# Kernel tuning notes

Hardware: AMD Instinct MI355X
Metric: run time of the kernel (lower is better)

Reference implementation:

```python
import jax, jax.numpy as jnp
import numpy as np

N_NODES = 100000
N_EDGES = 2000000
N_GRAPHS = 1024
HIDDEN = 32
LATENT = 8


def setup_inputs() -> dict:
    key = jax.random.key(0)
    ks = jax.random.split(key, 12)
    x = jax.random.normal(ks[0], (N_NODES, 1), dtype=jnp.float32)
    edge_index = jax.random.randint(ks[1], (2, N_EDGES), 0, N_NODES, dtype=jnp.int32)
    batch = jnp.sort(jax.random.randint(ks[2], (N_NODES,), 0, N_GRAPHS, dtype=jnp.int32))
    s = 0.1
    W = jax.random.normal(ks[3], (1, HIDDEN), dtype=jnp.float32) * s
    b = jax.random.normal(ks[4], (HIDDEN,), dtype=jnp.float32) * s
    w_mu = jax.random.normal(ks[5], (HIDDEN, LATENT), dtype=jnp.float32) * s
    b_mu = jax.random.normal(ks[6], (LATENT,), dtype=jnp.float32) * s
    w_lv = jax.random.normal(ks[7], (HIDDEN, LATENT), dtype=jnp.float32) * s
    b_lv = jax.random.normal(ks[8], (LATENT,), dtype=jnp.float32) * s
    w_dec = jax.random.normal(ks[9], (LATENT, 100), dtype=jnp.float32) * s
    b_dec = jax.random.normal(ks[10], (100,), dtype=jnp.float32) * s
    eps = jax.random.normal(ks[11], (N_GRAPHS, LATENT), dtype=jnp.float32)
    return {"x": x, "edge_index": edge_index, "batch": batch, "W": W, "b": b,
            "w_mu": w_mu, "b_mu": b_mu, "w_lv": w_lv, "b_lv": b_lv,
            "w_dec": w_dec, "b_dec": b_dec, "eps": eps}


def gcn_conv(x, edge_index, W, b):
    # PyG GCNConv: add self-loops, symmetric D^-1/2 (A+I) D^-1/2 normalization
    n = x.shape[0]
    loop = jnp.arange(n, dtype=edge_index.dtype)
    src = jnp.concatenate([edge_index[0], loop])
    dst = jnp.concatenate([edge_index[1], loop])
    deg = jax.ops.segment_sum(jnp.ones_like(dst, dtype=x.dtype), dst, num_segments=n)
    dinv = jnp.where(deg > 0, jax.lax.rsqrt(jnp.maximum(deg, 1.0)), 0.0)
    norm = dinv[src] * dinv[dst]          # [E+N]
    h = x @ W                              # [N, hidden] (tiny GEMM)
    msg = h[src] * norm[:, None]           # gather + scale (memory bound)
    out = jax.ops.segment_sum(msg, dst, num_segments=n)  # scatter-add
    return out + b


def reference(x, edge_index, batch, W, b, w_mu, b_mu, w_lv, b_lv, w_dec, b_dec, eps):
    G = eps.shape[0]
    h = jax.nn.relu(gcn_conv(x, edge_index, W, b))       # [N, hidden]
    sums = jax.ops.segment_sum(h, batch, num_segments=G)
    cnts = jax.ops.segment_sum(jnp.ones((h.shape[0],), h.dtype), batch, num_segments=G)
    pooled = sums / jnp.maximum(cnts, 1.0)[:, None]      # global_mean_pool [G, hidden]
    mu = pooled @ w_mu + b_mu                            # [G, latent]
    logvar = pooled @ w_lv + b_lv
    z = mu + eps * jnp.exp(0.5 * logvar)                 # reparam
    adj_logits = (z @ w_dec + b_dec).reshape(-1, 10, 10)
    adj = (jax.nn.sigmoid(adj_logits) > 0.5).astype(jnp.float32)
    return adj, mu, logvar
```

## Files before the change

kernel.cpp:

```cpp
#include <hip/hip_runtime.h>

#define HID 32
#define LAT 8
#define BSH 8
#define BUCK 256
#define CAPSH 13
#define CB 512
#define PB 512
#define PEV 16
#define PCHUNK (PB * PEV)

__device__ __forceinline__ double atomAddF64(double* p, double v) {
    return unsafeAtomicAdd(p, v);
}

__global__ void zero_kernel(unsigned* __restrict__ p, int n) {
    int i = blockIdx.x * blockDim.x + threadIdx.x;
    if (i < n) p[i] = 0;
}


__global__ __launch_bounds__(PB)
void place3_kernel(const unsigned* __restrict__ src, const unsigned* __restrict__ dst,
                   int E, int HBn,
                   unsigned* __restrict__ cursor, unsigned* __restrict__ csr) {
    __shared__ unsigned cnt[512];
    __shared__ unsigned gbase[512];
    uint4 dv[PEV / 4];
    unsigned rank[PEV];
    int tid = threadIdx.x;

    cnt[tid] = 0;
    __syncthreads();

    int E4 = E >> 2;
    int base4 = blockIdx.x * (PCHUNK / 4);
    #pragma unroll
    for (int k = 0; k < PEV / 4; k++) {
        int i4 = base4 + k * PB + tid;
        if (i4 < E4) {
            dv[k] = ((const uint4*)dst)[i4];
            rank[4 * k + 0] = atomicAdd(&cnt[dv[k].x >> BSH], 1u);
            rank[4 * k + 1] = atomicAdd(&cnt[dv[k].y >> BSH], 1u);
            rank[4 * k + 2] = atomicAdd(&cnt[dv[k].z >> BSH], 1u);
            rank[4 * k + 3] = atomicAdd(&cnt[dv[k].w >> BSH], 1u);
        }
    }
    __syncthreads();

    if (tid < HBn) {
        unsigned c = cnt[tid];
        gbase[tid] = c ? atomicAdd(&cursor[tid], c) : 0u;
    }
    __syncthreads();

    #pragma unroll
    for (int k = 0; k < PEV / 4; k++) {
        int i4 = base4 + k * PB + tid;
        if (i4 < E4) {
            uint4 sv = ((const uint4*)src)[i4];
            unsigned d, s, bin, r;
            d = dv[k].x; s = sv.x; bin = d >> BSH; r = gbase[bin] + rank[4 * k + 0];
            if (r < (1u << CAPSH)) csr[((size_t)bin << CAPSH) + r] = ((d & (BUCK - 1u)) << 17) | s;
            d = dv[k].y; s = sv.y; bin = d >> BSH; r = gbase[bin] + rank[4 * k + 1];
            if (r < (1u << CAPSH)) csr[((size_t)bin << CAPSH) + r] = ((d & (BUCK - 1u)) << 17) | s;
            d = dv[k].z; s = sv.z; bin = d >> BSH; r = gbase[bin] + rank[4 * k + 2];
            if (r < (1u << CAPSH)) csr[((size_t)bin << CAPSH) + r] = ((d & (BUCK - 1u)) << 17) | s;
            d = dv[k].w; s = sv.w; bin = d >> BSH; r = gbase[bin] + rank[4 * k + 3];
            if (r < (1u << CAPSH)) csr[((size_t)bin << CAPSH) + r] = ((d & (BUCK - 1u)) << 17) | s;
        }
    }
}

__global__ __launch_bounds__(CB)
void bdeg_kernel(const unsigned* __restrict__ cursor, const unsigned* __restrict__ csr,
                 int N, int G,
                 const float* __restrict__ x, const int* __restrict__ batch,
                 float* __restrict__ dinv, float* __restrict__ y32,
                 int* __restrict__ startArr) {
    int b = blockIdx.x;
    __shared__ unsigned cnt[BUCK];
    if (threadIdx.x < BUCK) cnt[threadIdx.x] = 0;
    __syncthreads();
    unsigned n = min(cursor[b], (unsigned)(1u << CAPSH));
    const unsigned* seg = csr + ((size_t)b << CAPSH);
    unsigned n4 = n >> 2;
    for (unsigned i = threadIdx.x; i < n4; i += CB) {
        uint4 v = ((const uint4*)seg)[i];
        atomicAdd(&cnt[v.x >> 17], 1u);
        atomicAdd(&cnt[v.y >> 17], 1u);
        atomicAdd(&cnt[v.z >> 17], 1u);
        atomicAdd(&cnt[v.w >> 17], 1u);
    }
    unsigned t = (n4 << 2) + threadIdx.x;
    if (t < n) atomicAdd(&cnt[seg[t] >> 17], 1u);
    __syncthreads();
    if (threadIdx.x < BUCK) {
        int node = (b << BSH) + threadIdx.x;
        if (node < N) {
            double dv = 1.0 / sqrt((double)(cnt[threadIdx.x] + 1));
            dinv[node] = (float)dv;
            y32[node] = (float)((double)x[node] * dv);
            int b1 = batch[node];
            if (node == 0) { for (int g = 0; g <= b1; g++) startArr[g] = 0; }
            else { int bp = batch[node - 1]; for (int g = bp + 1; g <= b1; g++) startArr[g] = node; }
            if (node == N - 1) { for (int g = b1 + 1; g <= G; g++) startArr[g] = N; }
        }
    }
}

__global__ __launch_bounds__(CB)
void bsum_kernel(const unsigned* __restrict__ cursor, const unsigned* __restrict__ csr,
                 int N,
                 const float* __restrict__ dinv, const float* __restrict__ y32,
                 double* __restrict__ acc) {
    int b = blockIdx.x;
    __shared__ double accs[BUCK];
    if (threadIdx.x < BUCK) accs[threadIdx.x] = 0.0;
    __syncthreads();
    unsigned n = min(cursor[b], (unsigned)(1u << CAPSH));
    const unsigned* seg = csr + ((size_t)b << CAPSH);
    unsigned n4 = n >> 2;
    for (unsigned i = threadIdx.x; i < n4; i += CB) {
        uint4 v = ((const uint4*)seg)[i];
        float ya = y32[v.x & 0x1FFFFu];
        float yb = y32[v.y & 0x1FFFFu];
        float yc = y32[v.z & 0x1FFFFu];
        float yd = y32[v.w & 0x1FFFFu];
        atomicAdd(&accs[v.x >> 17], (double)ya);
        atomicAdd(&accs[v.y >> 17], (double)yb);
        atomicAdd(&accs[v.z >> 17], (double)yc);
        atomicAdd(&accs[v.w >> 17], (double)yd);
    }
    unsigned t = (n4 << 2) + threadIdx.x;
    if (t < n) {
        unsigned v = seg[t];
        atomicAdd(&accs[v >> 17], (double)y32[v & 0x1FFFFu]);
    }
    __syncthreads();
    if (threadIdx.x < BUCK) {
        int node = (b << BSH) + threadIdx.x;
        if (node < N)
            acc[node] = (double)dinv[node] * ((double)y32[node] + accs[threadIdx.x]);
    }
}


__global__ void deg_kernel(const int* __restrict__ dst, int E, int* __restrict__ deg) {
    int e = blockIdx.x * blockDim.x + threadIdx.x;
    if (e < E) atomicAdd(&deg[dst[e]], 1);
}
__global__ void y_kernel(const float* __restrict__ x, const int* __restrict__ deg,
                         int N, double* __restrict__ y, double* __restrict__ acc) {
    int i = blockIdx.x * blockDim.x + threadIdx.x;
    if (i < N) {
        double dv = 1.0 / sqrt((double)(deg[i] + 1));
        double yi = (double)x[i] * dv;
        y[i] = yi; acc[i] = yi;
    }
}
__global__ void scatter_kernel(const int* __restrict__ ei, int E,
                               const double* __restrict__ y, double* __restrict__ acc) {
    int e = blockIdx.x * blockDim.x + threadIdx.x;
    if (e < E) atomAddF64(&acc[ei[E + e]], y[ei[e]]);
}
__global__ void finalize_kernel(const int* __restrict__ deg, int N, double* __restrict__ acc) {
    int i = blockIdx.x * blockDim.x + threadIdx.x;
    if (i < N) acc[i] *= 1.0 / sqrt((double)(deg[i] + 1));
}
__global__ void bounds_kernel(const int* __restrict__ batch, int N, int G,
                              int* __restrict__ start) {
    int i = blockIdx.x * blockDim.x + threadIdx.x;
    if (i >= N) return;
    int b1 = batch[i];
    if (i == 0) { for (int g = 0; g <= b1; g++) start[g] = 0; }
    else { int b0 = batch[i - 1]; for (int g = b0 + 1; g <= b1; g++) start[g] = i; }
    if (i == N - 1) { for (int g = b1 + 1; g <= G; g++) start[g] = N; }
}


__global__ __launch_bounds__(64)
void graph_kernel(const int* __restrict__ start, const double* __restrict__ acc,
                  const float* __restrict__ W, const float* __restrict__ b,
                  const float* __restrict__ w_mu, const float* __restrict__ b_mu,
                  const float* __restrict__ w_lv, const float* __restrict__ b_lv,
                  const float* __restrict__ w_dec, const float* __restrict__ b_dec,
                  const float* __restrict__ eps,
                  float* __restrict__ out, int G) {
    int g = blockIdx.x, lane = threadIdx.x;
    int s0 = start[g], s1 = start[g + 1];

    double hacc[HID];
    #pragma unroll
    for (int j = 0; j < HID; j++) hacc[j] = 0.0;

    for (int i = s0 + lane; i < s1; i += 64) {
        double s = acc[i];
        #pragma unroll
        for (int j = 0; j < HID; j++) {
            double h = (double)W[j] * s + (double)b[j];
            hacc[j] += (h > 0.0) ? h : 0.0;
        }
    }

    #pragma unroll
    for (int m = 1; m < 64; m <<= 1) {
        #pragma unroll
        for (int j = 0; j < HID; j++) hacc[j] += __shfl_xor(hacc[j], m, 64);
    }

    int c = s1 - s0;
    double denom = (c > 0) ? (double)c : 1.0;
    #pragma unroll
    for (int j = 0; j < HID; j++) hacc[j] /= denom;

    double mv = 0.0;
    if (lane < 16) {
        int l = lane & (LAT - 1);
        const float* wm = (lane < LAT) ? w_mu : w_lv;
        const float* bm = (lane < LAT) ? b_mu : b_lv;
        double a = (double)bm[l];
        #pragma unroll
        for (int j = 0; j < HID; j++) a += hacc[j] * (double)wm[j * LAT + l];
        mv = a;
        if (lane < LAT) out[(size_t)G * 100 + (size_t)g * LAT + l] = (float)a;
        else            out[(size_t)G * 100 + (size_t)G * LAT + (size_t)g * LAT + l] = (float)a;
    }

    double z[LAT];
    #pragma unroll
    for (int l = 0; l < LAT; l++) {
        double mu_l = __shfl(mv, l, 64);
        double lv_l = __shfl(mv, l + LAT, 64);
        z[l] = mu_l + (double)eps[(size_t)g * LAT + l] * exp(0.5 * lv_l);
    }

    for (int t = lane; t < 100; t += 64) {
        double lg = (double)b_dec[t];
        #pragma unroll
        for (int l = 0; l < LAT; l++) lg += z[l] * (double)w_dec[l * 100 + t];
        out[(size_t)g * 100 + t] = (lg > 0.0) ? 1.0f : 0.0f;
    }
}

extern "C" void kernel_launch(void* const* d_in, const int* in_sizes, int n_in,
                              void* d_out, int out_size, void* d_ws, size_t ws_size,
                              hipStream_t stream) {
    const float* x     = (const float*)d_in[0];
    const int*   ei    = (const int*)d_in[1];
    const int*   batch = (const int*)d_in[2];
    const float* W     = (const float*)d_in[3];
    const float* b     = (const float*)d_in[4];
    const float* w_mu  = (const float*)d_in[5];
    const float* b_mu  = (const float*)d_in[6];
    const float* w_lv  = (const float*)d_in[7];
    const float* b_lv  = (const float*)d_in[8];
    const float* w_dec = (const float*)d_in[9];
    const float* b_dec = (const float*)d_in[10];
    const float* eps   = (const float*)d_in[11];

    int N = in_sizes[0];
    int E = in_sizes[1] / 2;
    int G = in_sizes[11] / LAT;
    float* out = (float*)d_out;

    int HBn = (N + BUCK - 1) >> BSH;
    int NBp = (E + PCHUNK - 1) / PCHUNK;

    char* ws = (char*)d_ws;
    const int bs = 256;

    size_t off = 0;
    double*   acc    = (double*)(ws + off);   off += (size_t)N * 8;
    unsigned* csr    = (unsigned*)(ws + off); off += ((size_t)HBn << CAPSH) * 4;
    unsigned* cursor = (unsigned*)(ws + off); off += (size_t)HBn * 4;
    float*    dinv   = (float*)(ws + off);    off += (size_t)N * 4;
    float*    y32    = (float*)(ws + off);    off += (size_t)N * 4;
    int*      start  = (int*)(ws + off);      off += (size_t)(G + 1) * 4;
    size_t need = off;

    bool fast = (N <= 131072) && (HBn <= 512) && (ws_size >= need)
                && (E % 4 == 0)
                && ((long)E / HBn * 3 / 2 < (1L << CAPSH));

    if (fast) {
        zero_kernel<<<(HBn + bs - 1) / bs, bs, 0, stream>>>(cursor, HBn);
        place3_kernel<<<NBp, PB, 0, stream>>>((const unsigned*)ei, (const unsigned*)(ei + E),
                                              E, HBn, cursor, csr);
        bdeg_kernel<<<HBn, CB, 0, stream>>>(cursor, csr, N, G, x, batch, dinv, y32, start);
        bsum_kernel<<<HBn, CB, 0, stream>>>(cursor, csr, N, dinv, y32, acc);
    } else {
        size_t foff = 0;
        double* facc = (double*)(ws + foff); foff += (size_t)N * 8;
        double* fy   = (double*)(ws + foff); foff += (size_t)N * 8;
        int*    fdeg = (int*)(ws + foff);    foff += (size_t)N * 4;
        int*    fst  = (int*)(ws + foff);    foff += (size_t)(G + 1) * 4;
        acc = facc; start = fst;
        zero_kernel<<<(N + bs - 1) / bs, bs, 0, stream>>>((unsigned*)fdeg, N);
        deg_kernel<<<(E + bs - 1) / bs, bs, 0, stream>>>(ei + E, E, fdeg);
        y_kernel<<<(N + bs - 1) / bs, bs, 0, stream>>>(x, fdeg, N, fy, facc);
        scatter_kernel<<<(E + bs - 1) / bs, bs, 0, stream>>>(ei, E, fy, facc);
        finalize_kernel<<<(N + bs - 1) / bs, bs, 0, stream>>>(fdeg, N, facc);
        bounds_kernel<<<(N + bs - 1) / bs, bs, 0, stream>>>(batch, N, G, start);
    }

    graph_kernel<<<G, 64, 0, stream>>>(start, acc, W, b, w_mu, b_mu,
                                       w_lv, b_lv, w_dec, b_dec, eps, out, G);
}
```

Measured before the change: 52.29 us.

## Replace atomic-cursor fixed-capacity bucketing with histogram+scan compact CSR placement

```diff
diff --git a/kernel.cpp b/kernel.cpp
--- a/kernel.cpp
+++ b/kernel.cpp
@@ -4,11 +4,13 @@
 #define LAT 8
 #define BSH 8
 #define BUCK 256
-#define CAPSH 13
 #define CB 512
 #define PB 512
 #define PEV 16
 #define PCHUNK (PB * PEV)
+#define SCAN_BS 256
+#define SCAN_VPT 8
+#define SCAN_CHUNK (SCAN_BS * SCAN_VPT)
 
 __device__ __forceinline__ double atomAddF64(double* p, double v) {
     return unsafeAtomicAdd(p, v);
@@ -21,9 +23,85 @@
 
 
 __global__ __launch_bounds__(PB)
-void place3_kernel(const unsigned* __restrict__ src, const unsigned* __restrict__ dst,
-                   int E, int HBn,
-                   unsigned* __restrict__ cursor, unsigned* __restrict__ csr) {
+void hist_kernel(const unsigned* __restrict__ dst, int E, int NB, int HBn,
+                 unsigned* __restrict__ histMat) {
+    __shared__ unsigned cnt[512];
+    int tid = threadIdx.x;
+    cnt[tid] = 0;
+    __syncthreads();
+    int E4 = E >> 2;
+    int base4 = blockIdx.x * (PCHUNK / 4);
+    #pragma unroll
+    for (int k = 0; k < PEV / 4; k++) {
+        int i4 = base4 + k * PB + tid;
+        if (i4 < E4) {
+            uint4 d = ((const uint4*)dst)[i4];
+            atomicAdd(&cnt[d.x >> BSH], 1u);
+            atomicAdd(&cnt[d.y >> BSH], 1u);
+            atomicAdd(&cnt[d.z >> BSH], 1u);
+            atomicAdd(&cnt[d.w >> BSH], 1u);
+        }
+    }
+    __syncthreads();
+    if (tid < HBn) histMat[(size_t)tid * NB + blockIdx.x] = cnt[tid];
+}
+
+__global__ void scan_reduce(const unsigned* __restrict__ in, int M,
+                            unsigned* __restrict__ partials) {
+    int base = blockIdx.x * SCAN_CHUNK + threadIdx.x * SCAN_VPT;
+    unsigned s = 0;
+    #pragma unroll
+    for (int k = 0; k < SCAN_VPT; k++) { int i = base + k; if (i < M) s += in[i]; }
+    __shared__ unsigned red[SCAN_BS];
+    red[threadIdx.x] = s; __syncthreads();
+    for (int off = SCAN_BS / 2; off > 0; off >>= 1) {
+        if (threadIdx.x < off) red[threadIdx.x] += red[threadIdx.x + off];
+        __syncthreads();
+    }
+    if (threadIdx.x == 0) partials[blockIdx.x] = red[0];
+}
+
+__global__ void scan_partials(unsigned* __restrict__ partials, int SB) {
+    __shared__ unsigned lds[SCAN_BS];
+    unsigned v = (threadIdx.x < SB) ? partials[threadIdx.x] : 0;
+    lds[threadIdx.x] = v; __syncthreads();
+    for (int off = 1; off < SCAN_BS; off <<= 1) {
+        unsigned t = (threadIdx.x >= off) ? lds[threadIdx.x - off] : 0;
+        __syncthreads();
+        lds[threadIdx.x] += t;
+        __syncthreads();
+    }
+    if (threadIdx.x < SB) partials[threadIdx.x] = lds[threadIdx.x] - v;
+}
+
+__global__ void scan_apply(unsigned* __restrict__ data, int M,
+                           const unsigned* __restrict__ partials) {
+    int base = blockIdx.x * SCAN_CHUNK + threadIdx.x * SCAN_VPT;
+    unsigned vals[SCAN_VPT]; unsigned s = 0;
+    #pragma unroll
+    for (int k = 0; k < SCAN_VPT; k++) {
+        int i = base + k; vals[k] = (i < M) ? data[i] : 0; s += vals[k];
+    }
+    __shared__ unsigned lds[SCAN_BS];
+    lds[threadIdx.x] = s; __syncthreads();
+    for (int off = 1; off < SCAN_BS; off <<= 1) {
+        unsigned t = (threadIdx.x >= off) ? lds[threadIdx.x - off] : 0;
+        __syncthreads();
+        lds[threadIdx.x] += t;
+        __syncthreads();
+    }
+    unsigned excl = lds[threadIdx.x] - s + partials[blockIdx.x];
+    #pragma unroll
+    for (int k = 0; k < SCAN_VPT; k++) {
+        int i = base + k;
+        if (i < M) { unsigned v = vals[k]; data[i] = excl; excl += v; }
+    }
+}
+
+__global__ __launch_bounds__(PB)
+void place4_kernel(const unsigned* __restrict__ src, const unsigned* __restrict__ dst,
+                   int E, int NB, int HBn,
+                   const unsigned* __restrict__ S, unsigned* __restrict__ csr) {
     __shared__ unsigned cnt[512];
     __shared__ unsigned gbase[512];
     uint4 dv[PEV / 4];
@@ -48,10 +126,7 @@
     }
     __syncthreads();
 
-    if (tid < HBn) {
-        unsigned c = cnt[tid];
-        gbase[tid] = c ? atomicAdd(&cursor[tid], c) : 0u;
-    }
+    if (tid < HBn) gbase[tid] = S[(size_t)tid * NB + blockIdx.x];
     __syncthreads();
 
     #pragma unroll
@@ -59,22 +134,22 @@
         int i4 = base4 + k * PB + tid;
         if (i4 < E4) {
             uint4 sv = ((const uint4*)src)[i4];
-            unsigned d, s, bin, r;
-            d = dv[k].x; s = sv.x; bin = d >> BSH; r = gbase[bin] + rank[4 * k + 0];
-            if (r < (1u << CAPSH)) csr[((size_t)bin << CAPSH) + r] = ((d & (BUCK - 1u)) << 17) | s;
-            d = dv[k].y; s = sv.y; bin = d >> BSH; r = gbase[bin] + rank[4 * k + 1];
-            if (r < (1u << CAPSH)) csr[((size_t)bin << CAPSH) + r] = ((d & (BUCK - 1u)) << 17) | s;
-            d = dv[k].z; s = sv.z; bin = d >> BSH; r = gbase[bin] + rank[4 * k + 2];
-            if (r < (1u << CAPSH)) csr[((size_t)bin << CAPSH) + r] = ((d & (BUCK - 1u)) << 17) | s;
-            d = dv[k].w; s = sv.w; bin = d >> BSH; r = gbase[bin] + rank[4 * k + 3];
-            if (r < (1u << CAPSH)) csr[((size_t)bin << CAPSH) + r] = ((d & (BUCK - 1u)) << 17) | s;
+            unsigned d, bin;
+            d = dv[k].x; bin = d >> BSH;
+            csr[gbase[bin] + rank[4 * k + 0]] = ((d & (BUCK - 1u)) << 17) | sv.x;
+            d = dv[k].y; bin = d >> BSH;
+            csr[gbase[bin] + rank[4 * k + 1]] = ((d & (BUCK - 1u)) << 17) | sv.y;
+            d = dv[k].z; bin = d >> BSH;
+            csr[gbase[bin] + rank[4 * k + 2]] = ((d & (BUCK - 1u)) << 17) | sv.z;
+            d = dv[k].w; bin = d >> BSH;
+            csr[gbase[bin] + rank[4 * k + 3]] = ((d & (BUCK - 1u)) << 17) | sv.w;
         }
     }
 }
 
 __global__ __launch_bounds__(CB)
-void bdeg_kernel(const unsigned* __restrict__ cursor, const unsigned* __restrict__ csr,
-                 int N, int G,
+void bdeg_kernel(const unsigned* __restrict__ S, int NB, int HBn,
+                 const unsigned* __restrict__ csr, int E, int N, int G,
                  const float* __restrict__ x, const int* __restrict__ batch,
                  float* __restrict__ dinv, float* __restrict__ y32,
                  int* __restrict__ startArr) {
@@ -82,18 +157,23 @@
     __shared__ unsigned cnt[BUCK];
     if (threadIdx.x < BUCK) cnt[threadIdx.x] = 0;
     __syncthreads();
-    unsigned n = min(cursor[b], (unsigned)(1u << CAPSH));
-    const unsigned* seg = csr + ((size_t)b << CAPSH);
-    unsigned n4 = n >> 2;
+    unsigned s0 = S[(size_t)b * NB];
+    unsigned s1 = (b < HBn - 1) ? S[(size_t)(b + 1) * NB] : (unsigned)E;
+    unsigned ah = (4u - (s0 & 3u)) & 3u;
+    if (ah > s1 - s0) ah = s1 - s0;
+    if (threadIdx.x < ah) atomicAdd(&cnt[csr[s0 + threadIdx.x] >> 17], 1u);
+    unsigned a0 = s0 + ah;
+    unsigned n4 = (s1 - a0) >> 2;
+    const uint4* seg4 = (const uint4*)(csr + a0);
     for (unsigned i = threadIdx.x; i < n4; i += CB) {
-        uint4 v = ((const uint4*)seg)[i];
+        uint4 v = seg4[i];
         atomicAdd(&cnt[v.x >> 17], 1u);
         atomicAdd(&cnt[v.y >> 17], 1u);
         atomicAdd(&cnt[v.z >> 17], 1u);
         atomicAdd(&cnt[v.w >> 17], 1u);
     }
-    unsigned t = (n4 << 2) + threadIdx.x;
-    if (t < n) atomicAdd(&cnt[seg[t] >> 17], 1u);
+    unsigned t = a0 + (n4 << 2) + threadIdx.x;
+    if (t < s1) atomicAdd(&cnt[csr[t] >> 17], 1u);
     __syncthreads();
     if (threadIdx.x < BUCK) {
         int node = (b << BSH) + threadIdx.x;
@@ -110,19 +190,27 @@
 }
 
 __global__ __launch_bounds__(CB)
-void bsum_kernel(const unsigned* __restrict__ cursor, const unsigned* __restrict__ csr,
-                 int N,
+void bsum_kernel(const unsigned* __restrict__ S, int NB, int HBn,
+                 const unsigned* __restrict__ csr, int E, int N,
                  const float* __restrict__ dinv, const float* __restrict__ y32,
                  double* __restrict__ acc) {
     int b = blockIdx.x;
     __shared__ double accs[BUCK];
     if (threadIdx.x < BUCK) accs[threadIdx.x] = 0.0;
     __syncthreads();
-    unsigned n = min(cursor[b], (unsigned)(1u << CAPSH));
-    const unsigned* seg = csr + ((size_t)b << CAPSH);
-    unsigned n4 = n >> 2;
+    unsigned s0 = S[(size_t)b * NB];
+    unsigned s1 = (b < HBn - 1) ? S[(size_t)(b + 1) * NB] : (unsigned)E;
+    unsigned ah = (4u - (s0 & 3u)) & 3u;
+    if (ah > s1 - s0) ah = s1 - s0;
+    if (threadIdx.x < ah) {
+        unsigned v = csr[s0 + threadIdx.x];
+        atomicAdd(&accs[v >> 17], (double)y32[v & 0x1FFFFu]);
+    }
+    unsigned a0 = s0 + ah;
+    unsigned n4 = (s1 - a0) >> 2;
+    const uint4* seg4 = (const uint4*)(csr + a0);
     for (unsigned i = threadIdx.x; i < n4; i += CB) {
-        uint4 v = ((const uint4*)seg)[i];
+        uint4 v = seg4[i];
         float ya = y32[v.x & 0x1FFFFu];
         float yb = y32[v.y & 0x1FFFFu];
         float yc = y32[v.z & 0x1FFFFu];
@@ -132,9 +220,9 @@
         atomicAdd(&accs[v.z >> 17], (double)yc);
         atomicAdd(&accs[v.w >> 17], (double)yd);
     }
-    unsigned t = (n4 << 2) + threadIdx.x;
-    if (t < n) {
-        unsigned v = seg[t];
+    unsigned t = a0 + (n4 << 2) + threadIdx.x;
+    if (t < s1) {
+        unsigned v = csr[t];
         atomicAdd(&accs[v >> 17], (double)y32[v & 0x1FFFFu]);
     }
     __syncthreads();
@@ -265,30 +353,37 @@
     float* out = (float*)d_out;
 
     int HBn = (N + BUCK - 1) >> BSH;
-    int NBp = (E + PCHUNK - 1) / PCHUNK;
+    int NB  = (E + PCHUNK - 1) / PCHUNK;
+    long Ml = (long)HBn * NB;
+    int M = (int)Ml;
+    int SB = (int)((Ml + SCAN_CHUNK - 1) / SCAN_CHUNK);
 
     char* ws = (char*)d_ws;
     const int bs = 256;
 
     size_t off = 0;
-    double*   acc    = (double*)(ws + off);   off += (size_t)N * 8;
-    unsigned* csr    = (unsigned*)(ws + off); off += ((size_t)HBn << CAPSH) * 4;
-    unsigned* cursor = (unsigned*)(ws + off); off += (size_t)HBn * 4;
-    float*    dinv   = (float*)(ws + off);    off += (size_t)N * 4;
-    float*    y32    = (float*)(ws + off);    off += (size_t)N * 4;
-    int*      start  = (int*)(ws + off);      off += (size_t)(G + 1) * 4;
+    double*   acc   = (double*)(ws + off);   off += (size_t)N * 8;
+    unsigned* csr   = (unsigned*)(ws + off); off += (size_t)E * 4;
+    unsigned* hmat  = (unsigned*)(ws + off); off += (size_t)M * 4;
+    unsigned* parts = (unsigned*)(ws + off); off += (size_t)SCAN_BS * 4;
+    float*    dinv  = (float*)(ws + off);    off += (size_t)N * 4;
+    float*    y32   = (float*)(ws + off);    off += (size_t)N * 4;
+    int*      start = (int*)(ws + off);      off += (size_t)(G + 1) * 4;
     size_t need = off;
 
-    bool fast = (N <= 131072) && (HBn <= 512) && (ws_size >= need)
-                && (E % 4 == 0)
-                && ((long)E / HBn * 3 / 2 < (1L << CAPSH));
+    bool fast = (N <= 131072) && (HBn <= 512) && (SB <= SCAN_BS)
+                && (ws_size >= need) && (E % 4 == 0);
 
     if (fast) {
-        zero_kernel<<<(HBn + bs - 1) / bs, bs, 0, stream>>>(cursor, HBn);
-        place3_kernel<<<NBp, PB, 0, stream>>>((const unsigned*)ei, (const unsigned*)(ei + E),
-                                              E, HBn, cursor, csr);
-        bdeg_kernel<<<HBn, CB, 0, stream>>>(cursor, csr, N, G, x, batch, dinv, y32, start);
-        bsum_kernel<<<HBn, CB, 0, stream>>>(cursor, csr, N, dinv, y32, acc);
+        hist_kernel<<<NB, PB, 0, stream>>>((const unsigned*)(ei + E), E, NB, HBn, hmat);
+        scan_reduce<<<SB, SCAN_BS, 0, stream>>>(hmat, M, parts);
+        scan_partials<<<1, SCAN_BS, 0, stream>>>(parts, SB);
+        scan_apply<<<SB, SCAN_BS, 0, stream>>>(hmat, M, parts);
+        place4_kernel<<<NB, PB, 0, stream>>>((const unsigned*)ei, (const unsigned*)(ei + E),
+                                             E, NB, HBn, hmat, csr);
+        bdeg_kernel<<<HBn, CB, 0, stream>>>(hmat, NB, HBn, csr, E, N, G, x, batch,
+                                            dinv, y32, start);
+        bsum_kernel<<<HBn, CB, 0, stream>>>(hmat, NB, HBn, csr, E, N, dinv, y32, acc);
     } else {
         size_t foff = 0;
         double* facc = (double*)(ws + foff); foff += (size_t)N * 8;
```

Measured after the change: 59.17 us. 1.13x slower.

## Split edge bucketing into two-pass radix placement via coarse superbuckets

Applied to the files above, without the earlier changes.

```diff
diff --git a/kernel.cpp b/kernel.cpp
--- a/kernel.cpp
+++ b/kernel.cpp
@@ -5,10 +5,14 @@
 #define BSH 8
 #define BUCK 256
 #define CAPSH 13
+#define SSH 13
+#define CAP1SH 18
 #define CB 512
-#define PB 512
-#define PEV 16
-#define PCHUNK (PB * PEV)
+#define P1B 1024
+#define P1EV 32
+#define P1CHUNK (P1B * P1EV)
+#define P2B 512
+#define P2CHUNK 8192
 
 __device__ __forceinline__ double atomAddF64(double* p, double v) {
     return unsafeAtomicAdd(p, v);
@@ -20,54 +24,125 @@
 }
 
 
-__global__ __launch_bounds__(PB)
-void place3_kernel(const unsigned* __restrict__ src, const unsigned* __restrict__ dst,
-                   int E, int HBn,
-                   unsigned* __restrict__ cursor, unsigned* __restrict__ csr) {
-    __shared__ unsigned cnt[512];
-    __shared__ unsigned gbase[512];
-    uint4 dv[PEV / 4];
-    unsigned rank[PEV];
+__global__ __launch_bounds__(P1B)
+void place1_kernel(const unsigned* __restrict__ src, const unsigned* __restrict__ dst,
+                   int E, int nSup,
+                   unsigned* __restrict__ cursor1, unsigned* __restrict__ coarse) {
+    __shared__ unsigned cnt[16];
+    __shared__ unsigned gbase[16];
+    uint4 dv[P1EV / 4];
+    unsigned rank[P1EV];
     int tid = threadIdx.x;
-
-    cnt[tid] = 0;
+    if (tid < 16) cnt[tid] = 0;
     __syncthreads();
 
     int E4 = E >> 2;
-    int base4 = blockIdx.x * (PCHUNK / 4);
-    #pragma unroll
-    for (int k = 0; k < PEV / 4; k++) {
-        int i4 = base4 + k * PB + tid;
+    int base4 = blockIdx.x * (P1CHUNK / 4);
+    #pragma unroll
+    for (int k = 0; k < P1EV / 4; k++) {
+        int i4 = base4 + k * P1B + tid;
         if (i4 < E4) {
             dv[k] = ((const uint4*)dst)[i4];
-            rank[4 * k + 0] = atomicAdd(&cnt[dv[k].x >> BSH], 1u);
-            rank[4 * k + 1] = atomicAdd(&cnt[dv[k].y >> BSH], 1u);
-            rank[4 * k + 2] = atomicAdd(&cnt[dv[k].z >> BSH], 1u);
-            rank[4 * k + 3] = atomicAdd(&cnt[dv[k].w >> BSH], 1u);
-        }
-    }
-    __syncthreads();
-
-    if (tid < HBn) {
+            rank[4 * k + 0] = atomicAdd(&cnt[dv[k].x >> SSH], 1u);
+            rank[4 * k + 1] = atomicAdd(&cnt[dv[k].y >> SSH], 1u);
+            rank[4 * k + 2] = atomicAdd(&cnt[dv[k].z >> SSH], 1u);
+            rank[4 * k + 3] = atomicAdd(&cnt[dv[k].w >> SSH], 1u);
+        }
+    }
+    __syncthreads();
+
+    if (tid < nSup) {
         unsigned c = cnt[tid];
-        gbase[tid] = c ? atomicAdd(&cursor[tid], c) : 0u;
-    }
-    __syncthreads();
-
-    #pragma unroll
-    for (int k = 0; k < PEV / 4; k++) {
-        int i4 = base4 + k * PB + tid;
+        gbase[tid] = c ? atomicAdd(&cursor1[tid], c) : 0u;
+    }
+    __syncthreads();
+
+    #pragma unroll
+    for (int k = 0; k < P1EV / 4; k++) {
+        int i4 = base4 + k * P1B + tid;
         if (i4 < E4) {
             uint4 sv = ((const uint4*)src)[i4];
             unsigned d, s, bin, r;
-            d = dv[k].x; s = sv.x; bin = d >> BSH; r = gbase[bin] + rank[4 * k + 0];
-            if (r < (1u << CAPSH)) csr[((size_t)bin << CAPSH) + r] = ((d & (BUCK - 1u)) << 17) | s;
-            d = dv[k].y; s = sv.y; bin = d >> BSH; r = gbase[bin] + rank[4 * k + 1];
-            if (r < (1u << CAPSH)) csr[((size_t)bin << CAPSH) + r] = ((d & (BUCK - 1u)) << 17) | s;
-            d = dv[k].z; s = sv.z; bin = d >> BSH; r = gbase[bin] + rank[4 * k + 2];
-            if (r < (1u << CAPSH)) csr[((size_t)bin << CAPSH) + r] = ((d & (BUCK - 1u)) << 17) | s;
-            d = dv[k].w; s = sv.w; bin = d >> BSH; r = gbase[bin] + rank[4 * k + 3];
-            if (r < (1u << CAPSH)) csr[((size_t)bin << CAPSH) + r] = ((d & (BUCK - 1u)) << 17) | s;
+            d = dv[k].x; s = sv.x; bin = d >> SSH; r = gbase[bin] + rank[4 * k + 0];
+            if (r < (1u << CAP1SH)) coarse[((size_t)bin << CAP1SH) + r] = ((d & 8191u) << 17) | s;
+            d = dv[k].y; s = sv.y; bin = d >> SSH; r = gbase[bin] + rank[4 * k + 1];
+            if (r < (1u << CAP1SH)) coarse[((size_t)bin << CAP1SH) + r] = ((d & 8191u) << 17) | s;
+            d = dv[k].z; s = sv.z; bin = d >> SSH; r = gbase[bin] + rank[4 * k + 2];
+            if (r < (1u << CAP1SH)) coarse[((size_t)bin << CAP1SH) + r] = ((d & 8191u) << 17) | s;
+            d = dv[k].w; s = sv.w; bin = d >> SSH; r = gbase[bin] + rank[4 * k + 3];
+            if (r < (1u << CAP1SH)) coarse[((size_t)bin << CAP1SH) + r] = ((d & 8191u) << 17) | s;
+        }
+    }
+}
+
+__global__ __launch_bounds__(P2B)
+void place2b_kernel(const unsigned* __restrict__ cursor1, const unsigned* __restrict__ coarse,
+                    unsigned* __restrict__ cursor2, unsigned* __restrict__ csr) {
+    int sb = blockIdx.x >> 5;
+    unsigned chunk = blockIdx.x & 31u;
+    unsigned n1 = min(cursor1[sb], (unsigned)(1u << CAP1SH));
+    unsigned lo = chunk * (unsigned)P2CHUNK;
+    if (lo >= n1) return;
+    unsigned hi = min(lo + (unsigned)P2CHUNK, n1);
+
+    __shared__ unsigned cnt[64];
+    __shared__ unsigned gbase[32];
+    uint4 ev[4];
+    unsigned rank[16];
+    int tid = threadIdx.x;
+    if (tid < 64) cnt[tid] = 0;
+    __syncthreads();
+
+    const unsigned* seg = coarse + ((size_t)sb << CAP1SH);
+    #pragma unroll
+    for (int k = 0; k < 4; k++) {
+        unsigned i4 = (lo >> 2) + (unsigned)(k * P2B + tid);
+        unsigned e0 = i4 << 2;
+        if (e0 < hi) {
+            ev[k] = ((const uint4*)seg)[i4];
+            if (e0 + 0 < hi) rank[4 * k + 0] = atomicAdd(&cnt[(ev[k].x >> 17) >> 8], 1u);
+            if (e0 + 1 < hi) rank[4 * k + 1] = atomicAdd(&cnt[(ev[k].y >> 17) >> 8], 1u);
+            if (e0 + 2 < hi) rank[4 * k + 2] = atomicAdd(&cnt[(ev[k].z >> 17) >> 8], 1u);
+            if (e0 + 3 < hi) rank[4 * k + 3] = atomicAdd(&cnt[(ev[k].w >> 17) >> 8], 1u);
+        }
+    }
+    __syncthreads();
+
+    if (tid < 32) {
+        unsigned c = cnt[tid];
+        gbase[tid] = c ? atomicAdd(&cursor2[(sb << 5) + tid], c) : 0u;
+    }
+    __syncthreads();
+
+    #pragma unroll
+    for (int k = 0; k < 4; k++) {
+        unsigned e0 = ((lo >> 2) + (unsigned)(k * P2B + tid)) << 2;
+        if (e0 < hi) {
+            unsigned e, fb, r;
+            e = ev[k].x;
+            if (e0 + 0 < hi) {
+                fb = (e >> 17) >> 8; r = gbase[fb] + rank[4 * k + 0];
+                if (r < (1u << CAPSH))
+                    csr[(((size_t)(sb << 5) + fb) << CAPSH) + r] = (((e >> 17) & 255u) << 17) | (e & 0x1FFFFu);
+            }
+            e = ev[k].y;
+            if (e0 + 1 < hi) {
+                fb = (e >> 17) >> 8; r = gbase[fb] + rank[4 * k + 1];
+                if (r < (1u << CAPSH))
+                    csr[(((size_t)(sb << 5) + fb) << CAPSH) + r] = (((e >> 17) & 255u) << 17) | (e & 0x1FFFFu);
+            }
+            e = ev[k].z;
+            if (e0 + 2 < hi) {
+                fb = (e >> 17) >> 8; r = gbase[fb] + rank[4 * k + 2];
+                if (r < (1u << CAPSH))
+                    csr[(((size_t)(sb << 5) + fb) << CAPSH) + r] = (((e >> 17) & 255u) << 17) | (e & 0x1FFFFu);
+            }
+            e = ev[k].w;
+            if (e0 + 3 < hi) {
+                fb = (e >> 17) >> 8; r = gbase[fb] + rank[4 * k + 3];
+                if (r < (1u << CAPSH))
+                    csr[(((size_t)(sb << 5) + fb) << CAPSH) + r] = (((e >> 17) & 255u) << 17) | (e & 0x1FFFFu);
+            }
         }
     }
 }
@@ -264,31 +339,39 @@
     int G = in_sizes[11] / LAT;
     float* out = (float*)d_out;
 
-    int HBn = (N + BUCK - 1) >> BSH;
-    int NBp = (E + PCHUNK - 1) / PCHUNK;
+    int HBn  = (N + BUCK - 1) >> BSH;
+    int nSup = (N + 8191) >> SSH;
+    int NB1  = (E + P1CHUNK - 1) / P1CHUNK;
+    int NB2  = nSup << 5;
 
     char* ws = (char*)d_ws;
     const int bs = 256;
 
     size_t off = 0;
-    double*   acc    = (double*)(ws + off);   off += (size_t)N * 8;
-    unsigned* csr    = (unsigned*)(ws + off); off += ((size_t)HBn << CAPSH) * 4;
-    unsigned* cursor = (unsigned*)(ws + off); off += (size_t)HBn * 4;
-    float*    dinv   = (float*)(ws + off);    off += (size_t)N * 4;
-    float*    y32    = (float*)(ws + off);    off += (size_t)N * 4;
-    int*      start  = (int*)(ws + off);      off += (size_t)(G + 1) * 4;
+    double*   acc     = (double*)(ws + off);   off += (size_t)N * 8;
+    unsigned* csr     = (unsigned*)(ws + off); off += ((size_t)HBn << CAPSH) * 4;
+    unsigned* coarse  = (unsigned*)(ws + off); off += ((size_t)nSup << CAP1SH) * 4;
+    unsigned* cursors = (unsigned*)(ws + off); off += (size_t)(16 + (nSup << 5)) * 4;
+    float*    dinv    = (float*)(ws + off);    off += (size_t)N * 4;
+    float*    y32     = (float*)(ws + off);    off += (size_t)N * 4;
+    int*      start   = (int*)(ws + off);      off += (size_t)(G + 1) * 4;
     size_t need = off;
-
-    bool fast = (N <= 131072) && (HBn <= 512) && (ws_size >= need)
-                && (E % 4 == 0)
+    unsigned* cursor1 = cursors;
+    unsigned* cursor2 = cursors + 16;
+
+    bool fast = (N <= 106496) && (nSup <= 13) && (HBn <= (nSup << 5))
+                && (ws_size >= need) && (E % 4 == 0)
+                && ((long)E / nSup * 3 / 2 < (1L << CAP1SH))
                 && ((long)E / HBn * 3 / 2 < (1L << CAPSH));
 
     if (fast) {
-        zero_kernel<<<(HBn + bs - 1) / bs, bs, 0, stream>>>(cursor, HBn);
-        place3_kernel<<<NBp, PB, 0, stream>>>((const unsigned*)ei, (const unsigned*)(ei + E),
-                                              E, HBn, cursor, csr);
-        bdeg_kernel<<<HBn, CB, 0, stream>>>(cursor, csr, N, G, x, batch, dinv, y32, start);
-        bsum_kernel<<<HBn, CB, 0, stream>>>(cursor, csr, N, dinv, y32, acc);
+        int nz = 16 + (nSup << 5);
+        zero_kernel<<<1, 512, 0, stream>>>(cursors, nz);
+        place1_kernel<<<NB1, P1B, 0, stream>>>((const unsigned*)ei, (const unsigned*)(ei + E),
+                                               E, nSup, cursor1, coarse);
+        place2b_kernel<<<NB2, P2B, 0, stream>>>(cursor1, coarse, cursor2, csr);
+        bdeg_kernel<<<HBn, CB, 0, stream>>>(cursor2, csr, N, G, x, batch, dinv, y32, start);
+        bsum_kernel<<<HBn, CB, 0, stream>>>(cursor2, csr, N, dinv, y32, acc);
     } else {
         size_t foff = 0;
         double* facc = (double*)(ws + foff); foff += (size_t)N * 8;
```

After: 67.24 us. 28.6% more time.
